# Kernel optimization log

Measured on AMD Instinct MI355X. Metric: run time of the kernel, lower is better.

Reference implementation:

```python
import jax, jax.numpy as jnp
import numpy as np

KSIZE = 5  # local_range
MAX_DISP = 128


def _win_idx(n, k):
    # NATTEN-style clamped window: start = clamp(i - k//2, 0, n - k)
    start = jnp.clip(jnp.arange(n) - k // 2, 0, n - k)
    return start[:, None] + jnp.arange(k)[None, :]  # [n, k]


def _na2d(x, w_qkv, b_qkv, w_proj, b_proj, rpb, k=KSIZE):
    # x: [B, H, W, C], single head (num_heads=1), head_dim = C
    B, H, W, C = x.shape
    scale = C ** -0.5
    qkv = x @ w_qkv + b_qkv
    q, kk, v = jnp.split(qkv, 3, axis=-1)
    q = q * scale
    ih = _win_idx(H, k)  # [H, k]
    iw = _win_idx(W, k)  # [W, k]
    rows = ih[:, None, :, None]  # [H,1,k,1]
    cols = iw[None, :, None, :]  # [1,W,1,k]
    Kn = kk[:, rows, cols, :]    # [B,H,W,k,k,C]
    Vn = v[:, rows, cols, :]     # [B,H,W,k,k,C]
    # relative position bias index: (key_pos - query_pos) + (k-1) in [0, 2k-2]
    bi = ih - jnp.arange(H)[:, None] + (k - 1)  # [H,k]
    bj = iw - jnp.arange(W)[:, None] + (k - 1)  # [W,k]
    bias = rpb[bi[:, None, :, None], bj[None, :, None, :]]  # [H,W,k,k]
    logits = jnp.einsum('bhwc,bhwijc->bhwij', q, Kn) + bias
    a = jax.nn.softmax(logits.reshape(B, H, W, k * k), axis=-1).reshape(B, H, W, k, k)
    out = jnp.einsum('bhwij,bhwijc->bhwc', a, Vn)
    return out @ w_proj + b_proj


def _up2x(x):
    def resize(y, axis):
        n = y.shape[axis]
        m = 2 * n
        pos = jnp.arange(m, dtype=jnp.float32) * (n - 1) / (m - 1)
        i0 = jnp.floor(pos).astype(jnp.int32)
        i1 = jnp.minimum(i0 + 1, n - 1)
        w = (pos - i0.astype(jnp.float32))
        y0 = jnp.take(y, i0, axis=axis)
        y1 = jnp.take(y, i1, axis=axis)
        shp = [1] * y.ndim
        shp[axis] = m
        w = w.reshape(shp).astype(y.dtype)
        return y0 * (1 - w) + y1 * w
    return resize(resize(x, 1), 2)


def setup_inputs() -> dict:
    key = jax.random.key(0)
    ks = jax.random.split(key, 16)
    D, k = MAX_DISP, KSIZE
    B, H, W = 1, 24, 48

    def n(kk, shape, s=0.02):
        return jax.random.normal(kk, shape, dtype=jnp.float32) * s

    inp = {"attn": jax.random.normal(ks[0], (B, D // 4, H, W), dtype=jnp.float32)}
    i = 1
    for idx, c in [(1, D // 4), (2, D // 2), (3, D)]:
        inp[f"w_qkv{idx}"] = n(ks[i], (c, 3 * c)); i += 1
        inp[f"b_qkv{idx}"] = jnp.zeros((3 * c,), jnp.float32)
        inp[f"w_proj{idx}"] = n(ks[i], (c, c)); i += 1
        inp[f"b_proj{idx}"] = jnp.zeros((c,), jnp.float32)
        inp[f"rpb{idx}"] = n(ks[i], (2 * k - 1, 2 * k - 1)); i += 1
    inp["w_up1"] = n(ks[i], (D // 4, D // 2)); i += 1
    inp["b_up1"] = jnp.zeros((D // 2,), jnp.float32)
    inp["w_up2"] = n(ks[i], (D // 2, D)); i += 1
    inp["b_up2"] = jnp.zeros((D,), jnp.float32)
    return inp


def reference(attn, w_qkv1, b_qkv1, w_proj1, b_proj1, rpb1,
              w_qkv2, b_qkv2, w_proj2, b_proj2, rpb2,
              w_qkv3, b_qkv3, w_proj3, b_proj3, rpb3,
              w_up1, b_up1, w_up2, b_up2):
    x = jnp.transpose(attn, (0, 2, 3, 1))  # NHWC
    x = _na2d(x, w_qkv1, b_qkv1, w_proj1, b_proj1, rpb1)
    x = _up2x(x) @ w_up1 + b_up1           # 1x1 conv as channel matmul
    x = _na2d(x, w_qkv2, b_qkv2, w_proj2, b_proj2, rpb2)
    x = _up2x(x) @ w_up2 + b_up2
    x = _na2d(x, w_qkv3, b_qkv3, w_proj3, b_proj3, rpb3)
    return jnp.transpose(x, (0, 3, 1, 2))  # back to NCHW
```

## Files before the change

### kernel.cpp

```cpp
#include <hip/hip_runtime.h>
#include <math.h>


__global__ void compose2(const float* __restrict__ Wu1, const float* __restrict__ bu1,
                         const float* __restrict__ Wq2, const float* __restrict__ bq2,
                         const float* __restrict__ Wu2, const float* __restrict__ bu2,
                         const float* __restrict__ Wq3, const float* __restrict__ bq3,
                         float* __restrict__ Wc1, float* __restrict__ bc1,
                         float* __restrict__ Wc2, float* __restrict__ bc2) {
    int idx = blockIdx.x * blockDim.x + threadIdx.x;
    const int R1 = 33 * 192;
    if (idx < R1) {
        const int r = idx / 192;
        const int n = idx - r * 192;
        const float* wp = Wq2 + n;
        const float* a  = (r < 32) ? Wu1 + r * 64 : bu1;
        float s = 0.f;
        for (int k = 0; k < 64; ++k) s = fmaf(a[k], wp[(size_t)k * 192], s);
        if (r < 32) Wc1[r * 192 + n] = s;
        else        bc1[n] = s + bq2[n];
    } else {
        idx -= R1;
        if (idx >= 65 * 384) return;
        const int r = idx / 384;
        const int n = idx - r * 384;
        const float* wp = Wq3 + n;
        const float* a  = (r < 64) ? Wu2 + r * 128 : bu2;
        float s = 0.f;
        for (int k = 0; k < 128; ++k) s = fmaf(a[k], wp[(size_t)k * 384], s);
        if (r < 64) Wc2[r * 384 + n] = s;
        else        bc2[n] = s + bq3[n];
    }
}

template <int MT, int CHW>
__global__ void mm_bias(const float* __restrict__ A, const float* __restrict__ Wt,
                        const float* __restrict__ bias, float* __restrict__ out,
                        int M, int K, int N, int qcols, float qscale) {
    extern __shared__ float As[];
    const int m0 = blockIdx.x * MT;
    const int n  = threadIdx.x;
    if (CHW) {
        for (int idx = n; idx < MT * K; idx += blockDim.x) {
            const int r = idx / K;
            const int k = idx - r * K;
            As[idx] = A[(size_t)k * M + m0 + r];
        }
    } else {
        const float4* src = (const float4*)(A + (size_t)m0 * K);
        float4* dst = (float4*)As;
        for (int idx = n; idx < MT * K / 4; idx += blockDim.x) dst[idx] = src[idx];
    }
    __syncthreads();

    float acc[MT];
#pragma unroll
    for (int r = 0; r < MT; ++r) acc[r] = bias[n];
    for (int k = 0; k < K; k += 4) {
        const float* wp = Wt + (size_t)k * N + n;
        const float w0 = wp[0];
        const float w1 = wp[N];
        const float w2 = wp[2 * N];
        const float w3 = wp[3 * N];
#pragma unroll
        for (int r = 0; r < MT; ++r) {
            float4 a4 = *(const float4*)&As[r * K + k];
            acc[r] = fmaf(a4.x, w0, acc[r]);
            acc[r] = fmaf(a4.y, w1, acc[r]);
            acc[r] = fmaf(a4.z, w2, acc[r]);
            acc[r] = fmaf(a4.w, w3, acc[r]);
        }
    }
    if (n < qcols) {
#pragma unroll
        for (int r = 0; r < MT; ++r) acc[r] *= qscale;
    }
#pragma unroll
    for (int r = 0; r < MT; ++r) out[(size_t)(m0 + r) * N + n] = acc[r];
}

template <int BM, int BN, int NT, int TRANS, int UP>
__global__ __launch_bounds__(256) void gemm_rt(
        const float* __restrict__ A, const float* __restrict__ Wt,
        const float* __restrict__ bias, float* __restrict__ out,
        int M, int K, int N, int qcols, float qscale, int Hs, int Ws) {
    constexpr int BK = 16;
    constexpr int RT = BM / 16;
    constexpr int AIT = (BM * BK) / (4 * 256);
    constexpr int BIT = (BK * BN) / (4 * 256);
    __shared__ float As[BK][BM + 4];
    __shared__ float Bs[BK][BN + 4];
    const int tid = threadIdx.x;
    const int tn = tid >> 4;
    const int tm = tid & 15;
    const int m0 = blockIdx.x * BM;
    const int n0 = blockIdx.y * BN;

    const int sa_m = tid >> 2;
    const int sa_k = (tid & 3) << 2;

    const float* ybase[AIT][4];
    float uwh[AIT], uww[AIT];
    if (UP) {
        const int Wd = 2 * Ws, Hd = 2 * Hs;
#pragma unroll
        for (int i = 0; i < AIT; ++i) {
            const int row = m0 + sa_m + i * 64;
            const int h2 = row / Wd;
            const int w2 = row - h2 * Wd;
            const float ph = (float)h2 * (float)(Hs - 1) / (float)(Hd - 1);
            const int h0i = (int)ph;
            const int h1i = min(h0i + 1, Hs - 1);
            uwh[i] = ph - (float)h0i;
            const float pw = (float)w2 * (float)(Ws - 1) / (float)(Wd - 1);
            const int w0i = (int)pw;
            const int w1i = min(w0i + 1, Ws - 1);
            uww[i] = pw - (float)w0i;
            ybase[i][0] = A + ((size_t)h0i * Ws + w0i) * K;
            ybase[i][1] = A + ((size_t)h0i * Ws + w1i) * K;
            ybase[i][2] = A + ((size_t)h1i * Ws + w0i) * K;
            ybase[i][3] = A + ((size_t)h1i * Ws + w1i) * K;
        }
    }

    float acc[RT][NT];
#pragma unroll
    for (int r = 0; r < RT; ++r)
#pragma unroll
        for (int c = 0; c < NT; ++c) acc[r][c] = 0.f;

    for (int k0 = 0; k0 < K; k0 += BK) {
        float4 av[AIT];
#pragma unroll
        for (int i = 0; i < AIT; ++i) {
            if (UP) {
                const float4 v00 = *(const float4*)(ybase[i][0] + k0 + sa_k);
                const float4 v01 = *(const float4*)(ybase[i][1] + k0 + sa_k);
                const float4 v10 = *(const float4*)(ybase[i][2] + k0 + sa_k);
                const float4 v11 = *(const float4*)(ybase[i][3] + k0 + sa_k);
                const float wh = uwh[i], ww = uww[i];
                av[i].x = (v00.x * (1.f - wh) + v10.x * wh) * (1.f - ww) +
                          (v01.x * (1.f - wh) + v11.x * wh) * ww;
                av[i].y = (v00.y * (1.f - wh) + v10.y * wh) * (1.f - ww) +
                          (v01.y * (1.f - wh) + v11.y * wh) * ww;
                av[i].z = (v00.z * (1.f - wh) + v10.z * wh) * (1.f - ww) +
                          (v01.z * (1.f - wh) + v11.z * wh) * ww;
                av[i].w = (v00.w * (1.f - wh) + v10.w * wh) * (1.f - ww) +
                          (v01.w * (1.f - wh) + v11.w * wh) * ww;
            } else {
                av[i] = *(const float4*)(A + (size_t)(m0 + sa_m + i * 64) * K + k0 + sa_k);
            }
        }
        float4 bv[BIT];
#pragma unroll
        for (int i = 0; i < BIT; ++i) {
            const int f  = tid + i * 256;
            const int kl = f / (BN / 4);
            const int n4 = f - kl * (BN / 4);
            bv[i] = *(const float4*)(Wt + (size_t)(k0 + kl) * N + n0 + n4 * 4);
        }
        __syncthreads();
#pragma unroll
        for (int i = 0; i < AIT; ++i) {
            As[sa_k + 0][sa_m + i * 64] = av[i].x;
            As[sa_k + 1][sa_m + i * 64] = av[i].y;
            As[sa_k + 2][sa_m + i * 64] = av[i].z;
            As[sa_k + 3][sa_m + i * 64] = av[i].w;
        }
#pragma unroll
        for (int i = 0; i < BIT; ++i) {
            const int f  = tid + i * 256;
            const int kl = f / (BN / 4);
            const int n4 = f - kl * (BN / 4);
            *(float4*)&Bs[kl][n4 * 4] = bv[i];
        }
        __syncthreads();
#pragma unroll
        for (int kk = 0; kk < BK; ++kk) {
            float a[RT];
#pragma unroll
            for (int q = 0; q < RT / 4; ++q) {
                float4 t = *(const float4*)&As[kk][tm * RT + q * 4];
                a[q * 4 + 0] = t.x; a[q * 4 + 1] = t.y;
                a[q * 4 + 2] = t.z; a[q * 4 + 3] = t.w;
            }
            float b[NT];
#pragma unroll
            for (int q = 0; q < NT / 4; ++q) {
                float4 t = *(const float4*)&Bs[kk][tn * NT + q * 4];
                b[q * 4 + 0] = t.x; b[q * 4 + 1] = t.y;
                b[q * 4 + 2] = t.z; b[q * 4 + 3] = t.w;
            }
#pragma unroll
            for (int r = 0; r < RT; ++r)
#pragma unroll
                for (int c = 0; c < NT; ++c)
                    acc[r][c] = fmaf(a[r], b[c], acc[r][c]);
        }
    }

#pragma unroll
    for (int c = 0; c < NT; ++c) {
        const int n = n0 + tn * NT + c;
        const float bz = bias[n];
        const float sc = (n < qcols) ? qscale : 1.f;
#pragma unroll
        for (int r = 0; r < RT; ++r) acc[r][c] = (acc[r][c] + bz) * sc;
    }
    if (TRANS) {
#pragma unroll
        for (int c = 0; c < NT; ++c) {
            const int n = n0 + tn * NT + c;
            float* op = out + (size_t)n * M + m0 + tm * RT;
#pragma unroll
            for (int q = 0; q < RT / 4; ++q)
                *(float4*)(op + q * 4) = make_float4(acc[q * 4][c], acc[q * 4 + 1][c],
                                                     acc[q * 4 + 2][c], acc[q * 4 + 3][c]);
        }
    } else {
#pragma unroll
        for (int r = 0; r < RT; ++r) {
            float* op = out + (size_t)(m0 + tm * RT + r) * N + n0 + tn * NT;
#pragma unroll
            for (int q = 0; q < NT / 4; ++q)
                *(float4*)(op + q * 4) = make_float4(acc[r][q * 4], acc[r][q * 4 + 1],
                                                     acc[r][q * 4 + 2], acc[r][q * 4 + 3]);
        }
    }
}

template <int VPL>
__device__ inline void loadv(const float* __restrict__ p, float* d) {
    if constexpr (VPL == 2) {
        float2 t = *(const float2*)p;
        d[0] = t.x; d[1] = t.y;
    } else if constexpr (VPL == 4) {
        float4 t = *(const float4*)p;
        d[0] = t.x; d[1] = t.y; d[2] = t.z; d[3] = t.w;
    } else {
        float4 t0 = *(const float4*)p;
        float4 t1 = *(const float4*)(p + 4);
        d[0] = t0.x; d[1] = t0.y; d[2] = t0.z; d[3] = t0.w;
        d[4] = t1.x; d[5] = t1.y; d[6] = t1.z; d[7] = t1.w;
    }
}

template <int C, int TRANS>
__global__ __launch_bounds__(256) void na2d_proj(
        const float* __restrict__ qkv, const float* __restrict__ rpb,
        const float* __restrict__ Wp, const float* __restrict__ bp,
        float* __restrict__ out, int H, int W, int M) {
    constexpr int VPL = C / 16;
    constexpr int NT  = C / 16;
    __shared__ float att_s[16][C + 4];
    __shared__ float Bs[16][C];
    const int tid  = threadIdx.x;
    const int lane = tid & 63;
    const int g    = lane >> 4;
    const int li   = lane & 15;
    const int wave = tid >> 6;
    const int lp   = wave * 4 + g;
    const int pix  = blockIdx.x * 16 + lp;
    const int h = pix / W;
    const int w = pix - h * W;
    const int h0 = min(max(h - 2, 0), H - 5);
    const int w0 = min(max(w - 2, 0), W - 5);
    const int cb = li * VPL;
    const int bih = h0 - h + 4;
    const int biw = w0 - w + 4;

    float qf[VPL];
    loadv<VPL>(qkv + (size_t)pix * (3 * C) + cb, qf);

    float p[25];
#pragma unroll
    for (int jr = 0; jr < 5; ++jr) {
        const float* rowk = qkv + (size_t)((h0 + jr) * W + w0) * (3 * C) + C + cb;
        float kf[5][VPL];
#pragma unroll
        for (int jc = 0; jc < 5; ++jc) loadv<VPL>(rowk + jc * 3 * C, kf[jc]);
#pragma unroll
        for (int jc = 0; jc < 5; ++jc) {
            float s = qf[0] * kf[jc][0];
#pragma unroll
            for (int v = 1; v < VPL; ++v) s = fmaf(qf[v], kf[jc][v], s);
            p[jr * 5 + jc] = s;
        }
    }
#pragma unroll
    for (int jr = 0; jr < 5; ++jr)
#pragma unroll
        for (int jc = 0; jc < 5; ++jc) {
            const int j = jr * 5 + jc;
            float v = p[j];
            v += __shfl_xor(v, 1);
            v += __shfl_xor(v, 2);
            v += __shfl_xor(v, 4);
            v += __shfl_xor(v, 8);
            p[j] = v + rpb[(bih + jr) * 9 + (biw + jc)];
        }
    float mx = p[0];
#pragma unroll
    for (int j = 1; j < 25; ++j) mx = fmaxf(mx, p[j]);
    float sum = 0.f;
#pragma unroll
    for (int j = 0; j < 25; ++j) {
        p[j] = expf(p[j] - mx);
        sum += p[j];
    }
    const float inv = 1.f / sum;

    float a[VPL];
#pragma unroll
    for (int v = 0; v < VPL; ++v) a[v] = 0.f;
#pragma unroll
    for (int jr = 0; jr < 5; ++jr) {
        const float* rowv = qkv + (size_t)((h0 + jr) * W + w0) * (3 * C) + 2 * C + cb;
        float vf[5][VPL];
#pragma unroll
        for (int jc = 0; jc < 5; ++jc) loadv<VPL>(rowv + jc * 3 * C, vf[jc]);
#pragma unroll
        for (int jc = 0; jc < 5; ++jc)
#pragma unroll
            for (int v = 0; v < VPL; ++v) a[v] = fmaf(p[jr * 5 + jc], vf[jc][v], a[v]);
    }
#pragma unroll
    for (int v = 0; v < VPL; ++v) att_s[lp][cb + v] = a[v] * inv;

    const int tm = tid & 15;
    const int tn = tid >> 4;
    constexpr int WPT = C / 16;
    const int skl = tid >> 4;
    const int snn = (tid & 15) * WPT;
    float acc[NT];
#pragma unroll
    for (int c = 0; c < NT; ++c) acc[c] = bp[tn * NT + c];

    for (int k0 = 0; k0 < C; k0 += 16) {
        float tmp[WPT];
        {
            const float* src = Wp + (size_t)(k0 + skl) * C + snn;
#pragma unroll
            for (int t = 0; t < WPT; ++t) tmp[t] = src[t];
        }
        __syncthreads();
#pragma unroll
        for (int t = 0; t < WPT; ++t) Bs[skl][snn + t] = tmp[t];
        __syncthreads();
#pragma unroll
        for (int kk = 0; kk < 16; ++kk) {
            const float av = att_s[tm][k0 + kk];
            const float* bsp = &Bs[kk][tn * NT];
#pragma unroll
            for (int c = 0; c < NT; ++c) acc[c] = fmaf(av, bsp[c], acc[c]);
        }
    }

    const int m0 = blockIdx.x * 16;
    if (TRANS) {
#pragma unroll
        for (int c = 0; c < NT; ++c)
            out[(size_t)(tn * NT + c) * M + m0 + tm] = acc[c];
    } else {
        float* op = out + (size_t)(m0 + tm) * C + tn * NT;
#pragma unroll
        for (int c = 0; c < NT; ++c) op[c] = acc[c];
    }
}

extern "C" void kernel_launch(void* const* d_in, const int* in_sizes, int n_in,
                              void* d_out, int out_size, void* d_ws, size_t ws_size,
                              hipStream_t stream) {
    const float* attn    = (const float*)d_in[0];
    const float* w_qkv1  = (const float*)d_in[1];
    const float* b_qkv1  = (const float*)d_in[2];
    const float* w_proj1 = (const float*)d_in[3];
    const float* b_proj1 = (const float*)d_in[4];
    const float* rpb1    = (const float*)d_in[5];
    const float* w_qkv2  = (const float*)d_in[6];
    const float* b_qkv2  = (const float*)d_in[7];
    const float* w_proj2 = (const float*)d_in[8];
    const float* b_proj2 = (const float*)d_in[9];
    const float* rpb2    = (const float*)d_in[10];
    const float* w_qkv3  = (const float*)d_in[11];
    const float* b_qkv3  = (const float*)d_in[12];
    const float* w_proj3 = (const float*)d_in[13];
    const float* b_proj3 = (const float*)d_in[14];
    const float* rpb3    = (const float*)d_in[15];
    const float* w_up1   = (const float*)d_in[16];
    const float* b_up1   = (const float*)d_in[17];
    const float* w_up2   = (const float*)d_in[18];
    const float* b_up2   = (const float*)d_in[19];
    float* out = (float*)d_out;

    float* ws   = (float*)d_ws;
    float* bufB = ws + 2359296;
    float* bufD = bufB + 7077888;
    float* wc1  = bufD + 294912;
    float* bc1  = wc1 + 6144;
    float* wc2  = bc1 + 192;
    float* bc2  = wc2 + 24576;

    compose2<<<(33 * 192 + 65 * 384 + 255) / 256, 256, 0, stream>>>(
        w_up1, b_up1, w_qkv2, b_qkv2, w_up2, b_up2, w_qkv3, b_qkv3,
        wc1, bc1, wc2, bc2);

    {
        const int H = 24, W = 48, C = 32, M = H * W;
        mm_bias<16, 1><<<M / 16, 3 * C, 16 * C * 4, stream>>>(
            attn, w_qkv1, b_qkv1, bufB, M, C, 3 * C, C, 1.f / sqrtf((float)C));
        na2d_proj<32, 0><<<M / 16, 256, 0, stream>>>(
            bufB, rpb1, w_proj1, b_proj1, bufD, H, W, M);
    }
    {
        const int H = 48, W = 96, C = 64, M = H * W;
        gemm_rt<64, 64, 4, 0, 1><<<dim3(M / 64, 3), 256, 0, stream>>>(
            bufD, wc1, bc1, bufB, M, 32, 3 * C, C, 1.f / sqrtf((float)C), 24, 48);
        na2d_proj<64, 0><<<M / 16, 256, 0, stream>>>(
            bufB, rpb2, w_proj2, b_proj2, bufD, H, W, M);
    }
    {
        const int H = 96, W = 192, C = 128, M = H * W;
        gemm_rt<128, 128, 8, 0, 1><<<dim3(M / 128, 3), 256, 0, stream>>>(
            bufD, wc2, bc2, bufB, M, 64, 3 * C, C, 1.f / sqrtf((float)C), 48, 96);
        na2d_proj<128, 1><<<M / 16, 256, 0, stream>>>(
            bufB, rpb3, w_proj3, b_proj3, out, H, W, M);
    }
}
```

Before: 107.8 us.

## Fuse stage-1 QKV projection, neighborhood attention and output projection into one kernel

Replaces the stage-1 mm_bias QKV kernel and the na2d_proj kernel with a single kernel. Each block loads a 5x20 halo of input pixels into shared memory, computes QKV for the halo in place, runs the 5x5 neighborhood attention and applies the output projection. This removes one launch and the global round trip of the QKV buffer. The cost is recomputing QKV for halo pixels, and the grid is only 72 blocks with a large shared-memory footprint.

Result: slower. 111.3 us (+3.2%).

```diff
diff --git a/kernel.cpp b/kernel.cpp
--- a/kernel.cpp
+++ b/kernel.cpp
@@ -33,50 +33,127 @@
     }
 }
 
-template <int MT, int CHW>
-__global__ void mm_bias(const float* __restrict__ A, const float* __restrict__ Wt,
-                        const float* __restrict__ bias, float* __restrict__ out,
-                        int M, int K, int N, int qcols, float qscale) {
-    extern __shared__ float As[];
-    const int m0 = blockIdx.x * MT;
-    const int n  = threadIdx.x;
-    if (CHW) {
-        for (int idx = n; idx < MT * K; idx += blockDim.x) {
-            const int r = idx / K;
-            const int k = idx - r * K;
-            As[idx] = A[(size_t)k * M + m0 + r];
-        }
-    } else {
-        const float4* src = (const float4*)(A + (size_t)m0 * K);
-        float4* dst = (float4*)As;
-        for (int idx = n; idx < MT * K / 4; idx += blockDim.x) dst[idx] = src[idx];
+__global__ __launch_bounds__(256) void fused_s1(
+        const float* __restrict__ x,
+        const float* __restrict__ Wq,
+        const float* __restrict__ bq,
+        const float* __restrict__ rpb,
+        const float* __restrict__ Wp,
+        const float* __restrict__ bp,
+        float* __restrict__ y) {
+    const int H = 24, W = 48, M = 1152;
+    __shared__ float xh[100][32];
+    __shared__ float wq_s[32][96];
+    __shared__ float qkvh[100][100];
+    __shared__ float att_s[16][36];
+    __shared__ float wp_s[32][32];
+
+    const int tid  = threadIdx.x;
+    const int pix0 = blockIdx.x * 16;
+    const int hrow = pix0 / W;
+    const int wb   = pix0 - hrow * W;
+    const int r0   = min(max(hrow - 2, 0), H - 5);
+    const int c0   = wb - 2;
+
+    for (int i = tid; i < 32 * 96; i += 256) ((float*)wq_s)[i] = Wq[i];
+    for (int i = tid; i < 32 * 32; i += 256) ((float*)wp_s)[i] = Wp[i];
+    for (int i = tid; i < 3200; i += 256) {
+        const int c = i / 100;
+        const int s = i - c * 100;
+        const int ir = s / 20, jc = s - ir * 20;
+        const int col = c0 + jc;
+        float v = 0.f;
+        if (col >= 0 && col < W) v = x[(size_t)c * M + (r0 + ir) * W + col];
+        xh[s][c] = v;
     }
     __syncthreads();
 
-    float acc[MT];
-#pragma unroll
-    for (int r = 0; r < MT; ++r) acc[r] = bias[n];
-    for (int k = 0; k < K; k += 4) {
-        const float* wp = Wt + (size_t)k * N + n;
-        const float w0 = wp[0];
-        const float w1 = wp[N];
-        const float w2 = wp[2 * N];
-        const float w3 = wp[3 * N];
-#pragma unroll
-        for (int r = 0; r < MT; ++r) {
-            float4 a4 = *(const float4*)&As[r * K + k];
-            acc[r] = fmaf(a4.x, w0, acc[r]);
-            acc[r] = fmaf(a4.y, w1, acc[r]);
-            acc[r] = fmaf(a4.z, w2, acc[r]);
-            acc[r] = fmaf(a4.w, w3, acc[r]);
-        }
-    }
-    if (n < qcols) {
-#pragma unroll
-        for (int r = 0; r < MT; ++r) acc[r] *= qscale;
-    }
-#pragma unroll
-    for (int r = 0; r < MT; ++r) out[(size_t)(m0 + r) * N + n] = acc[r];
+    const float qscale = 0.17677669529663687f;
+    for (int i = tid; i < 100 * 24; i += 256) {
+        const int s  = i / 24;
+        const int n4 = (i - s * 24) * 4;
+        float4 acc = *(const float4*)&bq[n4];
+        for (int k = 0; k < 32; ++k) {
+            const float xv = xh[s][k];
+            const float4 wv = *(const float4*)&wq_s[k][n4];
+            acc.x = fmaf(xv, wv.x, acc.x);
+            acc.y = fmaf(xv, wv.y, acc.y);
+            acc.z = fmaf(xv, wv.z, acc.z);
+            acc.w = fmaf(xv, wv.w, acc.w);
+        }
+        if (n4 < 32) { acc.x *= qscale; acc.y *= qscale; acc.z *= qscale; acc.w *= qscale; }
+        *(float4*)&qkvh[s][n4] = acc;
+    }
+    __syncthreads();
+
+    const int lane = tid & 63;
+    const int g    = lane >> 4;
+    const int li   = lane & 15;
+    const int wave = tid >> 6;
+    const int lp   = wave * 4 + g;
+    const int w    = wb + lp;
+    const int w0p  = min(max(w - 2, 0), W - 5);
+    const int cs0  = w0p - c0;
+    const int cb   = li * 2;
+    const int sown = (hrow - r0) * 20 + (lp + 2);
+    const float q0 = qkvh[sown][cb];
+    const float q1 = qkvh[sown][cb + 1];
+    const int bih = r0 - hrow + 4;
+    const int biw = w0p - w + 4;
+
+    float p[25];
+#pragma unroll
+    for (int jr = 0; jr < 5; ++jr)
+#pragma unroll
+        for (int jc = 0; jc < 5; ++jc) {
+            const int s = jr * 20 + cs0 + jc;
+            p[jr * 5 + jc] = fmaf(q0, qkvh[s][32 + cb], q1 * qkvh[s][32 + cb + 1]);
+        }
+#pragma unroll
+    for (int j = 0; j < 25; ++j) {
+        float v = p[j];
+        v += __shfl_xor(v, 1);
+        v += __shfl_xor(v, 2);
+        v += __shfl_xor(v, 4);
+        v += __shfl_xor(v, 8);
+        p[j] = v + rpb[(bih + j / 5) * 9 + (biw + j % 5)];
+    }
+    float mx = p[0];
+#pragma unroll
+    for (int j = 1; j < 25; ++j) mx = fmaxf(mx, p[j]);
+    float sum = 0.f;
+#pragma unroll
+    for (int j = 0; j < 25; ++j) {
+        p[j] = expf(p[j] - mx);
+        sum += p[j];
+    }
+    const float inv = 1.f / sum;
+    float a0 = 0.f, a1 = 0.f;
+#pragma unroll
+    for (int jr = 0; jr < 5; ++jr)
+#pragma unroll
+        for (int jc = 0; jc < 5; ++jc) {
+            const int s = jr * 20 + cs0 + jc;
+            const float pj = p[jr * 5 + jc];
+            a0 = fmaf(pj, qkvh[s][64 + cb], a0);
+            a1 = fmaf(pj, qkvh[s][64 + cb + 1], a1);
+        }
+    att_s[lp][cb]     = a0 * inv;
+    att_s[lp][cb + 1] = a1 * inv;
+    __syncthreads();
+
+    const int tm = tid & 15;
+    const int tn = tid >> 4;
+    float acc0 = bp[tn * 2];
+    float acc1 = bp[tn * 2 + 1];
+    for (int k = 0; k < 32; ++k) {
+        const float av = att_s[tm][k];
+        acc0 = fmaf(av, wp_s[k][tn * 2], acc0);
+        acc1 = fmaf(av, wp_s[k][tn * 2 + 1], acc1);
+    }
+    float* op = y + (size_t)(pix0 + tm) * 32 + tn * 2;
+    op[0] = acc0;
+    op[1] = acc1;
 }
 
 template <int BM, int BN, int NT, int TRANS, int UP>
@@ -405,13 +482,9 @@
         w_up1, b_up1, w_qkv2, b_qkv2, w_up2, b_up2, w_qkv3, b_qkv3,
         wc1, bc1, wc2, bc2);
 
-    {
-        const int H = 24, W = 48, C = 32, M = H * W;
-        mm_bias<16, 1><<<M / 16, 3 * C, 16 * C * 4, stream>>>(
-            attn, w_qkv1, b_qkv1, bufB, M, C, 3 * C, C, 1.f / sqrtf((float)C));
-        na2d_proj<32, 0><<<M / 16, 256, 0, stream>>>(
-            bufB, rpb1, w_proj1, b_proj1, bufD, H, W, M);
-    }
+    fused_s1<<<72, 256, 0, stream>>>(attn, w_qkv1, b_qkv1, rpb1,
+                                     w_proj1, b_proj1, bufD);
+
     {
         const int H = 48, W = 96, C = 64, M = H * W;
         gemm_rt<64, 64, 4, 0, 1><<<dim3(M / 64, 3), 256, 0, stream>>>(
```
